# Kernel tuning notes

Measured on AMD Instinct MI355X. Metric: run time of the kernel, lower is better.

Reference implementation:

```python
import jax, jax.numpy as jnp
import numpy as np

N, E, NNZ, CIN, COUT = 100000, 25000, 1600000, 256, 256


def setup_inputs() -> dict:
    key = jax.random.key(0)
    k_x, k_v, k_e, k_w = jax.random.split(key, 4)
    X = jax.random.normal(k_x, (N, CIN), dtype=jnp.float32)
    v_idx = jax.random.randint(k_v, (NNZ,), 0, N)      # vertex of each incidence pair
    e_idx = jax.random.randint(k_e, (NNZ,), 0, E)      # hyperedge of each incidence pair
    # kaiming_normal_ on theta.weight: std = sqrt(2 / fan_in)
    W = jax.random.normal(k_w, (CIN, COUT), dtype=jnp.float32) * np.sqrt(2.0 / CIN)
    b = jnp.zeros((COUT,), dtype=jnp.float32)
    return {"X": X, "W": W, "b": b, "v_idx": v_idx, "e_idx": e_idx}


def reference(X, W, b, v_idx, e_idx):
    # theta: linear projection
    Xp = X @ W + b  # [N, COUT]

    # degrees (edge weights = 1)
    ones = jnp.ones((NNZ,), dtype=Xp.dtype)
    dv = jax.ops.segment_sum(ones, v_idx, num_segments=N)  # vertex degree
    de = jax.ops.segment_sum(ones, e_idx, num_segments=E)  # hyperedge degree
    dv_isqrt = jnp.where(dv > 0, jax.lax.rsqrt(jnp.maximum(dv, 1.0)), 0.0)
    de_inv = jnp.where(de > 0, 1.0 / jnp.maximum(de, 1.0), 0.0)

    # smoothing_with_HGNN: D_v^{-1/2} H D_e^{-1} H^T D_v^{-1/2} Xp
    Xs = Xp * dv_isqrt[:, None]                                            # [N, C]
    Ye = jax.ops.segment_sum(Xs[v_idx], e_idx, num_segments=E) * de_inv[:, None]  # [E, C]
    Zv = jax.ops.segment_sum(Ye[e_idx], v_idx, num_segments=N) * dv_isqrt[:, None]  # [N, C]

    # not is_last: ReLU; bn is None (use_bn=False); dropout identity at eval
    return jax.nn.relu(Zv)
```

## Files before the change

kernel.cpp:

```cpp
#include <hip/hip_runtime.h>
#include <hip/hip_bf16.h>

#define NV 100000
#define NE 25000
#define NNZ_ 1600000
#define CH 256
#define TS 4096
#define NB_T 391
#define EBINS 196
#define VBINS 196
#define HTOT (196*NB_T)
#define SEGCAP 9216
#define LDSK 264

typedef unsigned int u32;
typedef unsigned short u16;
typedef __attribute__((ext_vector_type(8))) short bf16x8;
typedef __attribute__((ext_vector_type(4))) float f32x4;

__device__ __forceinline__ float bf2f(u16 u){ return __uint_as_float(((u32)u)<<16); }
__device__ __forceinline__ u16 f2bf(float f){ __hip_bfloat16 h = __float2bfloat16(f); return *reinterpret_cast<u16*>(&h); }
__device__ __forceinline__ void acc4(float4& a, ushort4 u){
  a.x += bf2f(u.x); a.y += bf2f(u.y); a.z += bf2f(u.z); a.w += bf2f(u.w);
}

__global__ __launch_bounds__(256) void k_hist(const int* __restrict__ v_idx, const int* __restrict__ e_idx,
                       int* __restrict__ histE, int* __restrict__ histV){
  __shared__ int hE[EBINS], hV[VBINS];
  for (int i=threadIdx.x;i<EBINS;i+=256) hE[i]=0;
  for (int i=threadIdx.x;i<VBINS;i+=256) hV[i]=0;
  __syncthreads();
  int i0 = blockIdx.x*TS;
  int n = min(TS, NNZ_-i0);
  for (int k=threadIdx.x;k<n;k+=256){
    int e = e_idx[i0+k], v = v_idx[i0+k];
    atomicAdd(&hE[e>>7],1);
    atomicAdd(&hV[v>>9],1);
  }
  __syncthreads();
  for (int i=threadIdx.x;i<EBINS;i+=256) histE[i*NB_T+blockIdx.x]=hE[i];
  for (int i=threadIdx.x;i<VBINS;i+=256) histV[i*NB_T+blockIdx.x]=hV[i];
}

__global__ void k_scanA(const int* cnt, int n, int* off, int* bsum){
  __shared__ int buf[1024];
  int i = blockIdx.x*1024 + threadIdx.x;
  int x = (i<n) ? cnt[i] : 0;
  buf[threadIdx.x] = x;
  __syncthreads();
  #pragma unroll
  for (int d=1; d<1024; d<<=1){
    int t = (threadIdx.x>=d) ? buf[threadIdx.x-d] : 0;
    __syncthreads();
    buf[threadIdx.x] += t;
    __syncthreads();
  }
  if (i<n) off[i] = buf[threadIdx.x] - x;
  if (threadIdx.x==1023) bsum[blockIdx.x] = buf[1023];
}

__global__ void k_scanB(int* bsum, int nb){
  __shared__ int buf[128];
  int x = (threadIdx.x<nb) ? bsum[threadIdx.x] : 0;
  buf[threadIdx.x] = x;
  __syncthreads();
  #pragma unroll
  for (int d=1; d<128; d<<=1){
    int t = (threadIdx.x>=d) ? buf[threadIdx.x-d] : 0;
    __syncthreads();
    buf[threadIdx.x] += t;
    __syncthreads();
  }
  if (threadIdx.x<nb) bsum[threadIdx.x] = buf[threadIdx.x] - x;
}

__global__ void k_scanC2(int* off, const int* __restrict__ bsum, int n){
  int i = blockIdx.x*blockDim.x + threadIdx.x;
  if (i<n) off[i] += bsum[i>>10];
}

__global__ __launch_bounds__(256) void k_scat(const int* __restrict__ v_idx, const int* __restrict__ e_idx,
                       const int* __restrict__ baseE, const int* __restrict__ baseV,
                       u32* __restrict__ tmpE, u32* __restrict__ tmpV){
  __shared__ int bE[EBINS], bV[VBINS], cE[EBINS], cV[VBINS];
  for (int i=threadIdx.x;i<EBINS;i+=256){ bE[i]=baseE[i*NB_T+blockIdx.x]; cE[i]=0; }
  for (int i=threadIdx.x;i<VBINS;i+=256){ bV[i]=baseV[i*NB_T+blockIdx.x]; cV[i]=0; }
  __syncthreads();
  int i0 = blockIdx.x*TS;
  int n = min(TS, NNZ_-i0);
  for (int k=threadIdx.x;k<n;k+=256){
    int e = e_idx[i0+k], v = v_idx[i0+k];
    int be = e>>7, bv = v>>9;
    int r  = atomicAdd(&cE[be],1);
    tmpE[bE[be]+r] = ((u32)e<<17) | (u32)v;
    int r2 = atomicAdd(&cV[bv],1);
    tmpV[bV[bv]+r2] = ((u32)v<<15) | (u32)e;
  }
}

__global__ __launch_bounds__(256) void k_seg2e(const int* __restrict__ baseE, const u32* __restrict__ tmpE,
                        int* __restrict__ e_off, int* __restrict__ e_list){
  int seg = blockIdx.x;
  int s0 = baseE[seg*NB_T];
  int s1 = (seg+1<EBINS) ? baseE[(seg+1)*NB_T] : NNZ_;
  int len = s1 - s0;
  __shared__ u32 buf[SEGCAP];
  __shared__ int cnt[128], st[129];
  for (int i=threadIdx.x;i<128;i+=256) cnt[i]=0;
  __syncthreads();
  bool fit = (len <= SEGCAP);
  if (fit){
    for (int i=threadIdx.x;i<len;i+=256){ u32 p=tmpE[s0+i]; buf[i]=p; atomicAdd(&cnt[(p>>17)&127],1); }
  } else {
    for (int i=threadIdx.x;i<len;i+=256){ u32 p=tmpE[s0+i]; atomicAdd(&cnt[(p>>17)&127],1); }
  }
  __syncthreads();
  if (threadIdx.x==0){ int a=0; for (int i=0;i<128;i++){ st[i]=a; a+=cnt[i]; } st[128]=a; }
  __syncthreads();
  for (int i=threadIdx.x;i<128;i+=256){
    int e = seg*128 + i;
    if (e < NE) e_off[e] = s0 + st[i];
  }
  if (seg==EBINS-1 && threadIdx.x==0) e_off[NE] = NNZ_;
  for (int i=threadIdx.x;i<128;i+=256) cnt[i]=0;
  __syncthreads();
  if (fit){
    for (int i=threadIdx.x;i<len;i+=256){
      u32 p=buf[i]; int lb=(p>>17)&127; int r=atomicAdd(&cnt[lb],1);
      e_list[s0+st[lb]+r] = (int)(p & 0x1FFFFu);
    }
  } else {
    for (int i=threadIdx.x;i<len;i+=256){
      u32 p=tmpE[s0+i]; int lb=(p>>17)&127; int r=atomicAdd(&cnt[lb],1);
      e_list[s0+st[lb]+r] = (int)(p & 0x1FFFFu);
    }
  }
}

__global__ __launch_bounds__(256) void k_seg2v(const int* __restrict__ baseV, const u32* __restrict__ tmpV,
                        int* __restrict__ v_off, u16* __restrict__ v_list){
  int seg = blockIdx.x;
  int s0 = baseV[seg*NB_T];
  int s1 = (seg+1<VBINS) ? baseV[(seg+1)*NB_T] : NNZ_;
  int len = s1 - s0;
  __shared__ u32 buf[SEGCAP];
  __shared__ int cnt[512], st[513];
  for (int i=threadIdx.x;i<512;i+=256) cnt[i]=0;
  __syncthreads();
  bool fit = (len <= SEGCAP);
  if (fit){
    for (int i=threadIdx.x;i<len;i+=256){ u32 p=tmpV[s0+i]; buf[i]=p; atomicAdd(&cnt[(p>>15)&511],1); }
  } else {
    for (int i=threadIdx.x;i<len;i+=256){ u32 p=tmpV[s0+i]; atomicAdd(&cnt[(p>>15)&511],1); }
  }
  __syncthreads();
  if (threadIdx.x==0){ int a=0; for (int i=0;i<512;i++){ st[i]=a; a+=cnt[i]; } st[512]=a; }
  __syncthreads();
  for (int i=threadIdx.x;i<512;i+=256){
    int v = seg*512 + i;
    if (v < NV) v_off[v] = s0 + st[i];
  }
  if (seg==VBINS-1 && threadIdx.x==0) v_off[NV] = NNZ_;
  for (int i=threadIdx.x;i<512;i+=256) cnt[i]=0;
  __syncthreads();
  if (fit){
    for (int i=threadIdx.x;i<len;i+=256){
      u32 p=buf[i]; int lb=(p>>15)&511; int r=atomicAdd(&cnt[lb],1);
      v_list[s0+st[lb]+r] = (u16)(p & 0x7FFFu);
    }
  } else {
    for (int i=threadIdx.x;i<len;i+=256){
      u32 p=tmpV[s0+i]; int lb=(p>>15)&511; int r=atomicAdd(&cnt[lb],1);
      v_list[s0+st[lb]+r] = (u16)(p & 0x7FFFu);
    }
  }
}

__global__ void k_dvis(const int* __restrict__ v_off, float* __restrict__ dv_isqrt){
  int v = blockIdx.x*blockDim.x + threadIdx.x;
  if (v < NV){ int d = v_off[v+1]-v_off[v]; dv_isqrt[v] = d>0 ? rsqrtf((float)d) : 0.f; }
}

__global__ void k_xs(const float4* __restrict__ X4, const float* __restrict__ dv_isqrt,
                     ushort4* __restrict__ Xs4){
  int i = blockIdx.x*blockDim.x + threadIdx.x;
  int v = i >> 6;
  float w = dv_isqrt[v];
  float4 x = X4[i];
  ushort4 o;
  o.x = f2bf(x.x*w); o.y = f2bf(x.y*w); o.z = f2bf(x.z*w); o.w = f2bf(x.w*w);
  Xs4[i] = o;
}

__global__ void k_wh(const float* __restrict__ W, u16* __restrict__ Wh){
  __shared__ float tile[16][17];
  int bx=blockIdx.x, by=blockIdx.y;
  int tx=threadIdx.x, ty=threadIdx.y;
  tile[ty][tx] = W[(by*16+ty)*256 + bx*16+tx];
  __syncthreads();
  Wh[(bx*16+ty)*256 + by*16+tx] = f2bf(tile[tx][ty]);
}

__global__ __launch_bounds__(256) void k_tegemm(const int* __restrict__ e_off,
                     const int* __restrict__ e_list, const ushort4* __restrict__ Xs4,
                     const float* __restrict__ dv_isqrt, const u16* __restrict__ Wh,
                     float* __restrict__ tb, u16* __restrict__ Ue){
  __shared__ u16 lds[16][LDSK];
  int t = threadIdx.x, w = t>>6, lane = t&63;
  int e0 = blockIdx.x*16;

  for (int j=0;j<4;++j){
    int e = e0 + w*4 + j;
    int r = w*4 + j;
    float4 a0=make_float4(0,0,0,0), a1=make_float4(0,0,0,0);
    float ts = 0.f;
    if (e < NE){
      int beg = e_off[e], deg = e_off[e+1]-beg;
      int m = 0;
      for (; m+8 <= deg; m += 8){
        int v0=e_list[beg+m+0], v1=e_list[beg+m+1], v2=e_list[beg+m+2], v3=e_list[beg+m+3];
        int v4=e_list[beg+m+4], v5=e_list[beg+m+5], v6=e_list[beg+m+6], v7=e_list[beg+m+7];
        ushort4 u0=Xs4[(v0<<6)+lane], u1=Xs4[(v1<<6)+lane], u2=Xs4[(v2<<6)+lane], u3=Xs4[(v3<<6)+lane];
        ushort4 u4=Xs4[(v4<<6)+lane], u5=Xs4[(v5<<6)+lane], u6=Xs4[(v6<<6)+lane], u7=Xs4[(v7<<6)+lane];
        acc4(a0,u0); acc4(a1,u1); acc4(a0,u2); acc4(a1,u3);
        acc4(a0,u4); acc4(a1,u5); acc4(a0,u6); acc4(a1,u7);
        ts += dv_isqrt[v0]+dv_isqrt[v1]+dv_isqrt[v2]+dv_isqrt[v3]
            + dv_isqrt[v4]+dv_isqrt[v5]+dv_isqrt[v6]+dv_isqrt[v7];
      }
      for (; m<deg; ++m){
        int v = e_list[beg+m];
        ushort4 u = Xs4[(v<<6)+lane];
        acc4(a0,u);
        ts += dv_isqrt[v];
      }
      float dinv = deg>0 ? 1.f/(float)deg : 0.f;
      a0.x=(a0.x+a1.x)*dinv; a0.y=(a0.y+a1.y)*dinv; a0.z=(a0.z+a1.z)*dinv; a0.w=(a0.w+a1.w)*dinv;
      if (lane==0) tb[e] = ts*dinv;
    }
    ushort4 o;
    o.x=f2bf(a0.x); o.y=f2bf(a0.y); o.z=f2bf(a0.z); o.w=f2bf(a0.w);
    *reinterpret_cast<ushort4*>(&lds[r][lane*4]) = o;
  }
  __syncthreads();

  int rr = lane & 15, kg = lane >> 4;
  f32x4 acc0={0,0,0,0}, acc1={0,0,0,0}, acc2={0,0,0,0}, acc3={0,0,0,0};
  #pragma unroll
  for (int s=0; s<8; ++s){
    bf16x8 a = *reinterpret_cast<bf16x8*>(&lds[rr][s*32 + kg*8]);
    const u16* wb = &Wh[(size_t)((w*4)*16 + rr)*256 + s*32 + kg*8];
    bf16x8 b0 = *reinterpret_cast<const bf16x8*>(wb);
    bf16x8 b1 = *reinterpret_cast<const bf16x8*>(wb + 16*256);
    bf16x8 b2 = *reinterpret_cast<const bf16x8*>(wb + 32*256);
    bf16x8 b3 = *reinterpret_cast<const bf16x8*>(wb + 48*256);
    acc0 = __builtin_amdgcn_mfma_f32_16x16x32_bf16(a, b0, acc0, 0,0,0);
    acc1 = __builtin_amdgcn_mfma_f32_16x16x32_bf16(a, b1, acc1, 0,0,0);
    acc2 = __builtin_amdgcn_mfma_f32_16x16x32_bf16(a, b2, acc2, 0,0,0);
    acc3 = __builtin_amdgcn_mfma_f32_16x16x32_bf16(a, b3, acc3, 0,0,0);
  }
  __syncthreads();
  #pragma unroll
  for (int reg=0; reg<4; ++reg){
    int row = kg*4 + reg;
    lds[row][(w*4+0)*16 + rr] = f2bf(acc0[reg]);
    lds[row][(w*4+1)*16 + rr] = f2bf(acc1[reg]);
    lds[row][(w*4+2)*16 + rr] = f2bf(acc2[reg]);
    lds[row][(w*4+3)*16 + rr] = f2bf(acc3[reg]);
  }
  __syncthreads();
  int orow = t>>4, oseg = t&15;
  int e = e0 + orow;
  if (e < NE){
    uint4 d0 = *reinterpret_cast<uint4*>(&lds[orow][oseg*16]);
    uint4 d1 = *reinterpret_cast<uint4*>(&lds[orow][oseg*16+8]);
    *reinterpret_cast<uint4*>(&Ue[(size_t)e*256 + oseg*16])     = d0;
    *reinterpret_cast<uint4*>(&Ue[(size_t)e*256 + oseg*16 + 8]) = d1;
  }
}

__global__ __launch_bounds__(256) void k_zv(const int* __restrict__ v_off, const u16* __restrict__ v_list,
                    const ushort4* __restrict__ Ue4, const float* __restrict__ tb,
                    const float* __restrict__ dv_isqrt, const float4* __restrict__ b4,
                    float4* __restrict__ out4){
  int v = blockIdx.x*4 + (threadIdx.x>>6);
  if (v >= NV) return;
  int lane = threadIdx.x & 63;
  int base = v_off[v];
  int deg = v_off[v+1] - base;
  float4 a0 = make_float4(0,0,0,0), a1 = make_float4(0,0,0,0);
  float sb0 = 0.f, sb1 = 0.f;
  int m = 0;
  for (; m+8 <= deg; m += 8){
    int e0=v_list[base+m+0], e1=v_list[base+m+1], e2=v_list[base+m+2], e3=v_list[base+m+3];
    int e4=v_list[base+m+4], e5=v_list[base+m+5], e6=v_list[base+m+6], e7=v_list[base+m+7];
    ushort4 u0=Ue4[(e0<<6)+lane], u1=Ue4[(e1<<6)+lane], u2=Ue4[(e2<<6)+lane], u3=Ue4[(e3<<6)+lane];
    ushort4 u4=Ue4[(e4<<6)+lane], u5=Ue4[(e5<<6)+lane], u6=Ue4[(e6<<6)+lane], u7=Ue4[(e7<<6)+lane];
    acc4(a0,u0); acc4(a1,u1); acc4(a0,u2); acc4(a1,u3);
    acc4(a0,u4); acc4(a1,u5); acc4(a0,u6); acc4(a1,u7);
    sb0 += tb[e0]+tb[e2]+tb[e4]+tb[e6];
    sb1 += tb[e1]+tb[e3]+tb[e5]+tb[e7];
  }
  for (; m<deg; ++m){
    int e = v_list[base+m];
    ushort4 u = Ue4[(e<<6)+lane];
    acc4(a0,u);
    sb0 += tb[e];
  }
  float4 acc;
  acc.x=a0.x+a1.x; acc.y=a0.y+a1.y; acc.z=a0.z+a1.z; acc.w=a0.w+a1.w;
  float w = dv_isqrt[v];
  float sw = (sb0+sb1)*w;
  float4 bb = b4[lane];
  float4 o;
  o.x = fmaxf(0.f, fmaf(sw, bb.x, acc.x*w));
  o.y = fmaxf(0.f, fmaf(sw, bb.y, acc.y*w));
  o.z = fmaxf(0.f, fmaf(sw, bb.z, acc.z*w));
  o.w = fmaxf(0.f, fmaf(sw, bb.w, acc.w*w));
  out4[(v<<6)+lane] = o;
}

extern "C" void kernel_launch(void* const* d_in, const int* in_sizes, int n_in,
                              void* d_out, int out_size, void* d_ws, size_t ws_size,
                              hipStream_t stream) {
  const float* X = (const float*)d_in[0];
  const float* W = (const float*)d_in[1];
  const float* b = (const float*)d_in[2];
  const int* v_idx = (const int*)d_in[3];
  const int* e_idx = (const int*)d_in[4];
  float* out = (float*)d_out;

  char* p = (char*)d_ws;
  auto alloc = [&](size_t bytes)->void*{
    void* r = (void*)p; p += (bytes + 255) & ~(size_t)255; return r;
  };
  int* histE      = (int*)alloc((size_t)HTOT*4);
  int* histV      = (int*)alloc((size_t)HTOT*4);
  int* bsumE      = (int*)alloc(128*4);
  int* bsumV      = (int*)alloc(128*4);
  int* e_off      = (int*)alloc((size_t)(NE+1)*4);
  int* v_off      = (int*)alloc((size_t)(NV+1)*4);
  float* dv_isqrt = (float*)alloc((size_t)NV*4);
  float* tb       = (float*)alloc((size_t)NE*4);
  u32* tmpE       = (u32*)alloc((size_t)NNZ_*4);
  u32* tmpV       = (u32*)alloc((size_t)NNZ_*4);
  int* e_list     = (int*)alloc((size_t)NNZ_*4);
  u16* v_list     = (u16*)alloc((size_t)NNZ_*2);
  u16* Wh         = (u16*)alloc((size_t)CH*CH*2);
  u16* Ue         = (u16*)tmpE;
  u16* Xs         = (u16*)d_out;

  const int nbS = (HTOT+1023)/1024;

  k_hist<<<NB_T,256,0,stream>>>(v_idx,e_idx,histE,histV);
  k_scanA<<<nbS,1024,0,stream>>>(histE,HTOT,histE,bsumE);
  k_scanA<<<nbS,1024,0,stream>>>(histV,HTOT,histV,bsumV);
  k_scanB<<<1,128,0,stream>>>(bsumE,nbS);
  k_scanB<<<1,128,0,stream>>>(bsumV,nbS);
  k_scanC2<<<(HTOT+255)/256,256,0,stream>>>(histE,bsumE,HTOT);
  k_scanC2<<<(HTOT+255)/256,256,0,stream>>>(histV,bsumV,HTOT);
  k_scat<<<NB_T,256,0,stream>>>(v_idx,e_idx,histE,histV,tmpE,tmpV);
  k_seg2e<<<EBINS,256,0,stream>>>(histE,tmpE,e_off,e_list);
  k_seg2v<<<VBINS,256,0,stream>>>(histV,tmpV,v_off,v_list);

  k_dvis<<<(NV+255)/256,256,0,stream>>>(v_off, dv_isqrt);
  k_xs<<<(NV*64)/256,256,0,stream>>>((const float4*)X, dv_isqrt, (ushort4*)Xs);
  k_wh<<<dim3(16,16),dim3(16,16),0,stream>>>(W, Wh);
  k_tegemm<<<(NE+15)/16,256,0,stream>>>(e_off,e_list,(const ushort4*)Xs,dv_isqrt,Wh,tb,Ue);
  k_zv<<<(NV+3)/4,256,0,stream>>>(v_off,v_list,(const ushort4*)Ue,tb,dv_isqrt,(const float4*)b,(float4*)out);
}
```

Before: 369.7 us.

## Merge paired scan/sort/prep launches, add nontemporal hints, two vertices per wave

Merges the separate E/V scan, segment-sort, degree and weight-convert kernels into combined launches, which cuts the launch count and the idle gaps between small kernels. It adds nontemporal loads and stores for streaming index, X and output traffic. The final gather kernel now has each wave process two vertices at once, so more independent loads are in flight. The cost is higher register pressure in the gather kernel and load imbalance when the two vertices have different degrees.

```diff
diff --git a/kernel.cpp b/kernel.cpp
--- a/kernel.cpp
+++ b/kernel.cpp
@@ -33,7 +33,8 @@
   int i0 = blockIdx.x*TS;
   int n = min(TS, NNZ_-i0);
   for (int k=threadIdx.x;k<n;k+=256){
-    int e = e_idx[i0+k], v = v_idx[i0+k];
+    int e = __builtin_nontemporal_load(&e_idx[i0+k]);
+    int v = __builtin_nontemporal_load(&v_idx[i0+k]);
     atomicAdd(&hE[e>>7],1);
     atomicAdd(&hV[v>>9],1);
   }
@@ -42,10 +43,16 @@
   for (int i=threadIdx.x;i<VBINS;i+=256) histV[i*NB_T+blockIdx.x]=hV[i];
 }
 
-__global__ void k_scanA(const int* cnt, int n, int* off, int* bsum){
+__global__ void k_scanA2(int* __restrict__ histE, int* __restrict__ histV,
+                         int* __restrict__ bsumE, int* __restrict__ bsumV){
   __shared__ int buf[1024];
-  int i = blockIdx.x*1024 + threadIdx.x;
-  int x = (i<n) ? cnt[i] : 0;
+  int half = gridDim.x >> 1;
+  int sel = blockIdx.x >= half;
+  int blk = sel ? blockIdx.x - half : blockIdx.x;
+  int* data = sel ? histV : histE;
+  int* bsum = sel ? bsumV : bsumE;
+  int i = blk*1024 + threadIdx.x;
+  int x = (i<HTOT) ? data[i] : 0;
   buf[threadIdx.x] = x;
   __syncthreads();
   #pragma unroll
@@ -55,28 +62,35 @@
     buf[threadIdx.x] += t;
     __syncthreads();
   }
-  if (i<n) off[i] = buf[threadIdx.x] - x;
-  if (threadIdx.x==1023) bsum[blockIdx.x] = buf[1023];
-}
-
-__global__ void k_scanB(int* bsum, int nb){
-  __shared__ int buf[128];
-  int x = (threadIdx.x<nb) ? bsum[threadIdx.x] : 0;
-  buf[threadIdx.x] = x;
+  if (i<HTOT) data[i] = buf[threadIdx.x] - x;
+  if (threadIdx.x==1023) bsum[blk] = buf[1023];
+}
+
+__global__ void k_scanB2(int* __restrict__ bsumE, int* __restrict__ bsumV, int nb){
+  __shared__ int bufE[128], bufV[128];
+  int tid = threadIdx.x;
+  int isV = tid >= 128;
+  int* bsum = isV ? bsumV : bsumE;
+  int* buf  = isV ? bufV  : bufE;
+  int t = tid & 127;
+  int x = (t<nb) ? bsum[t] : 0;
+  buf[t] = x;
   __syncthreads();
   #pragma unroll
   for (int d=1; d<128; d<<=1){
-    int t = (threadIdx.x>=d) ? buf[threadIdx.x-d] : 0;
-    __syncthreads();
-    buf[threadIdx.x] += t;
-    __syncthreads();
-  }
-  if (threadIdx.x<nb) bsum[threadIdx.x] = buf[threadIdx.x] - x;
-}
-
-__global__ void k_scanC2(int* off, const int* __restrict__ bsum, int n){
+    int tmp = (t>=d) ? buf[t-d] : 0;
+    __syncthreads();
+    buf[t] += tmp;
+    __syncthreads();
+  }
+  if (t<nb) bsum[t] = buf[t] - x;
+}
+
+__global__ void k_scanC2(int* __restrict__ histE, int* __restrict__ histV,
+                         const int* __restrict__ bsumE, const int* __restrict__ bsumV){
   int i = blockIdx.x*blockDim.x + threadIdx.x;
-  if (i<n) off[i] += bsum[i>>10];
+  if (i < HTOT) histE[i] += bsumE[i>>10];
+  else if (i < 2*HTOT){ int j = i-HTOT; histV[j] += bsumV[j>>10]; }
 }
 
 __global__ __launch_bounds__(256) void k_scat(const int* __restrict__ v_idx, const int* __restrict__ e_idx,
@@ -89,7 +103,8 @@
   int i0 = blockIdx.x*TS;
   int n = min(TS, NNZ_-i0);
   for (int k=threadIdx.x;k<n;k+=256){
-    int e = e_idx[i0+k], v = v_idx[i0+k];
+    int e = __builtin_nontemporal_load(&e_idx[i0+k]);
+    int v = __builtin_nontemporal_load(&v_idx[i0+k]);
     int be = e>>7, bv = v>>9;
     int r  = atomicAdd(&cE[be],1);
     tmpE[bE[be]+r] = ((u32)e<<17) | (u32)v;
@@ -98,107 +113,109 @@
   }
 }
 
-__global__ __launch_bounds__(256) void k_seg2e(const int* __restrict__ baseE, const u32* __restrict__ tmpE,
-                        int* __restrict__ e_off, int* __restrict__ e_list){
-  int seg = blockIdx.x;
-  int s0 = baseE[seg*NB_T];
-  int s1 = (seg+1<EBINS) ? baseE[(seg+1)*NB_T] : NNZ_;
-  int len = s1 - s0;
-  __shared__ u32 buf[SEGCAP];
-  __shared__ int cnt[128], st[129];
-  for (int i=threadIdx.x;i<128;i+=256) cnt[i]=0;
-  __syncthreads();
-  bool fit = (len <= SEGCAP);
-  if (fit){
-    for (int i=threadIdx.x;i<len;i+=256){ u32 p=tmpE[s0+i]; buf[i]=p; atomicAdd(&cnt[(p>>17)&127],1); }
-  } else {
-    for (int i=threadIdx.x;i<len;i+=256){ u32 p=tmpE[s0+i]; atomicAdd(&cnt[(p>>17)&127],1); }
-  }
-  __syncthreads();
-  if (threadIdx.x==0){ int a=0; for (int i=0;i<128;i++){ st[i]=a; a+=cnt[i]; } st[128]=a; }
-  __syncthreads();
-  for (int i=threadIdx.x;i<128;i+=256){
-    int e = seg*128 + i;
-    if (e < NE) e_off[e] = s0 + st[i];
-  }
-  if (seg==EBINS-1 && threadIdx.x==0) e_off[NE] = NNZ_;
-  for (int i=threadIdx.x;i<128;i+=256) cnt[i]=0;
-  __syncthreads();
-  if (fit){
-    for (int i=threadIdx.x;i<len;i+=256){
-      u32 p=buf[i]; int lb=(p>>17)&127; int r=atomicAdd(&cnt[lb],1);
-      e_list[s0+st[lb]+r] = (int)(p & 0x1FFFFu);
-    }
-  } else {
-    for (int i=threadIdx.x;i<len;i+=256){
-      u32 p=tmpE[s0+i]; int lb=(p>>17)&127; int r=atomicAdd(&cnt[lb],1);
-      e_list[s0+st[lb]+r] = (int)(p & 0x1FFFFu);
-    }
-  }
-}
-
-__global__ __launch_bounds__(256) void k_seg2v(const int* __restrict__ baseV, const u32* __restrict__ tmpV,
+__global__ __launch_bounds__(256) void k_seg2(const int* __restrict__ baseE, const u32* __restrict__ tmpE,
+                        int* __restrict__ e_off, int* __restrict__ e_list,
+                        const int* __restrict__ baseV, const u32* __restrict__ tmpV,
                         int* __restrict__ v_off, u16* __restrict__ v_list){
-  int seg = blockIdx.x;
-  int s0 = baseV[seg*NB_T];
-  int s1 = (seg+1<VBINS) ? baseV[(seg+1)*NB_T] : NNZ_;
-  int len = s1 - s0;
   __shared__ u32 buf[SEGCAP];
   __shared__ int cnt[512], st[513];
-  for (int i=threadIdx.x;i<512;i+=256) cnt[i]=0;
-  __syncthreads();
-  bool fit = (len <= SEGCAP);
-  if (fit){
-    for (int i=threadIdx.x;i<len;i+=256){ u32 p=tmpV[s0+i]; buf[i]=p; atomicAdd(&cnt[(p>>15)&511],1); }
+  if (blockIdx.x < EBINS){
+    int seg = blockIdx.x;
+    int s0 = baseE[seg*NB_T];
+    int s1 = (seg+1<EBINS) ? baseE[(seg+1)*NB_T] : NNZ_;
+    int len = s1 - s0;
+    for (int i=threadIdx.x;i<128;i+=256) cnt[i]=0;
+    __syncthreads();
+    bool fit = (len <= SEGCAP);
+    if (fit){
+      for (int i=threadIdx.x;i<len;i+=256){ u32 p=tmpE[s0+i]; buf[i]=p; atomicAdd(&cnt[(p>>17)&127],1); }
+    } else {
+      for (int i=threadIdx.x;i<len;i+=256){ u32 p=tmpE[s0+i]; atomicAdd(&cnt[(p>>17)&127],1); }
+    }
+    __syncthreads();
+    if (threadIdx.x==0){ int a=0; for (int i=0;i<128;i++){ st[i]=a; a+=cnt[i]; } st[128]=a; }
+    __syncthreads();
+    for (int i=threadIdx.x;i<128;i+=256){
+      int e = seg*128 + i;
+      if (e < NE) e_off[e] = s0 + st[i];
+    }
+    if (seg==EBINS-1 && threadIdx.x==0) e_off[NE] = NNZ_;
+    for (int i=threadIdx.x;i<128;i+=256) cnt[i]=0;
+    __syncthreads();
+    if (fit){
+      for (int i=threadIdx.x;i<len;i+=256){
+        u32 p=buf[i]; int lb=(p>>17)&127; int r=atomicAdd(&cnt[lb],1);
+        e_list[s0+st[lb]+r] = (int)(p & 0x1FFFFu);
+      }
+    } else {
+      for (int i=threadIdx.x;i<len;i+=256){
+        u32 p=tmpE[s0+i]; int lb=(p>>17)&127; int r=atomicAdd(&cnt[lb],1);
+        e_list[s0+st[lb]+r] = (int)(p & 0x1FFFFu);
+      }
+    }
   } else {
-    for (int i=threadIdx.x;i<len;i+=256){ u32 p=tmpV[s0+i]; atomicAdd(&cnt[(p>>15)&511],1); }
-  }
-  __syncthreads();
-  if (threadIdx.x==0){ int a=0; for (int i=0;i<512;i++){ st[i]=a; a+=cnt[i]; } st[512]=a; }
-  __syncthreads();
-  for (int i=threadIdx.x;i<512;i+=256){
-    int v = seg*512 + i;
-    if (v < NV) v_off[v] = s0 + st[i];
-  }
-  if (seg==VBINS-1 && threadIdx.x==0) v_off[NV] = NNZ_;
-  for (int i=threadIdx.x;i<512;i+=256) cnt[i]=0;
-  __syncthreads();
-  if (fit){
-    for (int i=threadIdx.x;i<len;i+=256){
-      u32 p=buf[i]; int lb=(p>>15)&511; int r=atomicAdd(&cnt[lb],1);
-      v_list[s0+st[lb]+r] = (u16)(p & 0x7FFFu);
-    }
+    int seg = blockIdx.x - EBINS;
+    int s0 = baseV[seg*NB_T];
+    int s1 = (seg+1<VBINS) ? baseV[(seg+1)*NB_T] : NNZ_;
+    int len = s1 - s0;
+    for (int i=threadIdx.x;i<512;i+=256) cnt[i]=0;
+    __syncthreads();
+    bool fit = (len <= SEGCAP);
+    if (fit){
+      for (int i=threadIdx.x;i<len;i+=256){ u32 p=tmpV[s0+i]; buf[i]=p; atomicAdd(&cnt[(p>>15)&511],1); }
+    } else {
+      for (int i=threadIdx.x;i<len;i+=256){ u32 p=tmpV[s0+i]; atomicAdd(&cnt[(p>>15)&511],1); }
+    }
+    __syncthreads();
+    if (threadIdx.x==0){ int a=0; for (int i=0;i<512;i++){ st[i]=a; a+=cnt[i]; } st[512]=a; }
+    __syncthreads();
+    for (int i=threadIdx.x;i<512;i+=256){
+      int v = seg*512 + i;
+      if (v < NV) v_off[v] = s0 + st[i];
+    }
+    if (seg==VBINS-1 && threadIdx.x==0) v_off[NV] = NNZ_;
+    for (int i=threadIdx.x;i<512;i+=256) cnt[i]=0;
+    __syncthreads();
+    if (fit){
+      for (int i=threadIdx.x;i<len;i+=256){
+        u32 p=buf[i]; int lb=(p>>15)&511; int r=atomicAdd(&cnt[lb],1);
+        v_list[s0+st[lb]+r] = (u16)(p & 0x7FFFu);
+      }
+    } else {
+      for (int i=threadIdx.x;i<len;i+=256){
+        u32 p=tmpV[s0+i]; int lb=(p>>15)&511; int r=atomicAdd(&cnt[lb],1);
+        v_list[s0+st[lb]+r] = (u16)(p & 0x7FFFu);
+      }
+    }
+  }
+}
+
+__global__ void k_prep(const int* __restrict__ v_off, float* __restrict__ dv_isqrt,
+                       const float* __restrict__ W, u16* __restrict__ Wh){
+  const int nb_dv = (NV+255)/256;
+  if ((int)blockIdx.x < nb_dv){
+    int v = blockIdx.x*256 + threadIdx.x;
+    if (v < NV){ int d = v_off[v+1]-v_off[v]; dv_isqrt[v] = d>0 ? rsqrtf((float)d) : 0.f; }
   } else {
-    for (int i=threadIdx.x;i<len;i+=256){
-      u32 p=tmpV[s0+i]; int lb=(p>>15)&511; int r=atomicAdd(&cnt[lb],1);
-      v_list[s0+st[lb]+r] = (u16)(p & 0x7FFFu);
-    }
-  }
-}
-
-__global__ void k_dvis(const int* __restrict__ v_off, float* __restrict__ dv_isqrt){
-  int v = blockIdx.x*blockDim.x + threadIdx.x;
-  if (v < NV){ int d = v_off[v+1]-v_off[v]; dv_isqrt[v] = d>0 ? rsqrtf((float)d) : 0.f; }
-}
-
-__global__ void k_xs(const float4* __restrict__ X4, const float* __restrict__ dv_isqrt,
+    __shared__ float tile[16][17];
+    int idx = blockIdx.x - nb_dv;
+    int bx = idx & 15, by = idx >> 4;
+    int tx = threadIdx.x & 15, ty = threadIdx.x >> 4;
+    tile[ty][tx] = W[(by*16+ty)*256 + bx*16+tx];
+    __syncthreads();
+    Wh[(bx*16+ty)*256 + by*16+tx] = f2bf(tile[tx][ty]);
+  }
+}
+
+__global__ void k_xs(const f32x4* __restrict__ X4, const float* __restrict__ dv_isqrt,
                      ushort4* __restrict__ Xs4){
   int i = blockIdx.x*blockDim.x + threadIdx.x;
   int v = i >> 6;
   float w = dv_isqrt[v];
-  float4 x = X4[i];
+  f32x4 x = __builtin_nontemporal_load(&X4[i]);
   ushort4 o;
-  o.x = f2bf(x.x*w); o.y = f2bf(x.y*w); o.z = f2bf(x.z*w); o.w = f2bf(x.w*w);
+  o.x = f2bf(x[0]*w); o.y = f2bf(x[1]*w); o.z = f2bf(x[2]*w); o.w = f2bf(x[3]*w);
   Xs4[i] = o;
-}
-
-__global__ void k_wh(const float* __restrict__ W, u16* __restrict__ Wh){
-  __shared__ float tile[16][17];
-  int bx=blockIdx.x, by=blockIdx.y;
-  int tx=threadIdx.x, ty=threadIdx.y;
-  tile[ty][tx] = W[(by*16+ty)*256 + bx*16+tx];
-  __syncthreads();
-  Wh[(bx*16+ty)*256 + by*16+tx] = f2bf(tile[tx][ty]);
 }
 
 __global__ __launch_bounds__(256) void k_tegemm(const int* __restrict__ e_off,
@@ -282,41 +299,76 @@
                     const ushort4* __restrict__ Ue4, const float* __restrict__ tb,
                     const float* __restrict__ dv_isqrt, const float4* __restrict__ b4,
                     float4* __restrict__ out4){
-  int v = blockIdx.x*4 + (threadIdx.x>>6);
-  if (v >= NV) return;
-  int lane = threadIdx.x & 63;
-  int base = v_off[v];
-  int deg = v_off[v+1] - base;
-  float4 a0 = make_float4(0,0,0,0), a1 = make_float4(0,0,0,0);
-  float sb0 = 0.f, sb1 = 0.f;
+  int w = threadIdx.x>>6, lane = threadIdx.x&63;
+  int vA = blockIdx.x*8 + w*2;
+  int vB = vA + 1;
+  int baseA = v_off[vA], degA = v_off[vA+1]-baseA;
+  int baseB = v_off[vB], degB = v_off[vB+1]-baseB;
+  const float4 z = make_float4(0,0,0,0);
+  float4 a0=z, a1=z, c0=z, c1=z;
+  float sbA=0.f, sbB=0.f;
+  int mc = min(degA, degB);
   int m = 0;
-  for (; m+8 <= deg; m += 8){
-    int e0=v_list[base+m+0], e1=v_list[base+m+1], e2=v_list[base+m+2], e3=v_list[base+m+3];
-    int e4=v_list[base+m+4], e5=v_list[base+m+5], e6=v_list[base+m+6], e7=v_list[base+m+7];
+  for (; m+8 <= mc; m += 8){
+    int eA0=v_list[baseA+m+0], eA1=v_list[baseA+m+1], eA2=v_list[baseA+m+2], eA3=v_list[baseA+m+3];
+    int eA4=v_list[baseA+m+4], eA5=v_list[baseA+m+5], eA6=v_list[baseA+m+6], eA7=v_list[baseA+m+7];
+    int eB0=v_list[baseB+m+0], eB1=v_list[baseB+m+1], eB2=v_list[baseB+m+2], eB3=v_list[baseB+m+3];
+    int eB4=v_list[baseB+m+4], eB5=v_list[baseB+m+5], eB6=v_list[baseB+m+6], eB7=v_list[baseB+m+7];
+    ushort4 uA0=Ue4[(eA0<<6)+lane], uA1=Ue4[(eA1<<6)+lane], uA2=Ue4[(eA2<<6)+lane], uA3=Ue4[(eA3<<6)+lane];
+    ushort4 uA4=Ue4[(eA4<<6)+lane], uA5=Ue4[(eA5<<6)+lane], uA6=Ue4[(eA6<<6)+lane], uA7=Ue4[(eA7<<6)+lane];
+    ushort4 uB0=Ue4[(eB0<<6)+lane], uB1=Ue4[(eB1<<6)+lane], uB2=Ue4[(eB2<<6)+lane], uB3=Ue4[(eB3<<6)+lane];
+    ushort4 uB4=Ue4[(eB4<<6)+lane], uB5=Ue4[(eB5<<6)+lane], uB6=Ue4[(eB6<<6)+lane], uB7=Ue4[(eB7<<6)+lane];
+    acc4(a0,uA0); acc4(a1,uA1); acc4(a0,uA2); acc4(a1,uA3);
+    acc4(a0,uA4); acc4(a1,uA5); acc4(a0,uA6); acc4(a1,uA7);
+    acc4(c0,uB0); acc4(c1,uB1); acc4(c0,uB2); acc4(c1,uB3);
+    acc4(c0,uB4); acc4(c1,uB5); acc4(c0,uB6); acc4(c1,uB7);
+    sbA += tb[eA0]+tb[eA1]+tb[eA2]+tb[eA3]+tb[eA4]+tb[eA5]+tb[eA6]+tb[eA7];
+    sbB += tb[eB0]+tb[eB1]+tb[eB2]+tb[eB3]+tb[eB4]+tb[eB5]+tb[eB6]+tb[eB7];
+  }
+  int mA = m;
+  for (; mA+8 <= degA; mA += 8){
+    int e0=v_list[baseA+mA+0], e1=v_list[baseA+mA+1], e2=v_list[baseA+mA+2], e3=v_list[baseA+mA+3];
+    int e4=v_list[baseA+mA+4], e5=v_list[baseA+mA+5], e6=v_list[baseA+mA+6], e7=v_list[baseA+mA+7];
     ushort4 u0=Ue4[(e0<<6)+lane], u1=Ue4[(e1<<6)+lane], u2=Ue4[(e2<<6)+lane], u3=Ue4[(e3<<6)+lane];
     ushort4 u4=Ue4[(e4<<6)+lane], u5=Ue4[(e5<<6)+lane], u6=Ue4[(e6<<6)+lane], u7=Ue4[(e7<<6)+lane];
     acc4(a0,u0); acc4(a1,u1); acc4(a0,u2); acc4(a1,u3);
     acc4(a0,u4); acc4(a1,u5); acc4(a0,u6); acc4(a1,u7);
-    sb0 += tb[e0]+tb[e2]+tb[e4]+tb[e6];
-    sb1 += tb[e1]+tb[e3]+tb[e5]+tb[e7];
-  }
-  for (; m<deg; ++m){
-    int e = v_list[base+m];
-    ushort4 u = Ue4[(e<<6)+lane];
-    acc4(a0,u);
-    sb0 += tb[e];
-  }
-  float4 acc;
-  acc.x=a0.x+a1.x; acc.y=a0.y+a1.y; acc.z=a0.z+a1.z; acc.w=a0.w+a1.w;
-  float w = dv_isqrt[v];
-  float sw = (sb0+sb1)*w;
+    sbA += tb[e0]+tb[e1]+tb[e2]+tb[e3]+tb[e4]+tb[e5]+tb[e6]+tb[e7];
+  }
+  for (; mA<degA; ++mA){
+    int e = v_list[baseA+mA];
+    acc4(a0, Ue4[(e<<6)+lane]);
+    sbA += tb[e];
+  }
+  int mB = m;
+  for (; mB+8 <= degB; mB += 8){
+    int e0=v_list[baseB+mB+0], e1=v_list[baseB+mB+1], e2=v_list[baseB+mB+2], e3=v_list[baseB+mB+3];
+    int e4=v_list[baseB+mB+4], e5=v_list[baseB+mB+5], e6=v_list[baseB+mB+6], e7=v_list[baseB+mB+7];
+    ushort4 u0=Ue4[(e0<<6)+lane], u1=Ue4[(e1<<6)+lane], u2=Ue4[(e2<<6)+lane], u3=Ue4[(e3<<6)+lane];
+    ushort4 u4=Ue4[(e4<<6)+lane], u5=Ue4[(e5<<6)+lane], u6=Ue4[(e6<<6)+lane], u7=Ue4[(e7<<6)+lane];
+    acc4(c0,u0); acc4(c1,u1); acc4(c0,u2); acc4(c1,u3);
+    acc4(c0,u4); acc4(c1,u5); acc4(c0,u6); acc4(c1,u7);
+    sbB += tb[e0]+tb[e1]+tb[e2]+tb[e3]+tb[e4]+tb[e5]+tb[e6]+tb[e7];
+  }
+  for (; mB<degB; ++mB){
+    int e = v_list[baseB+mB];
+    acc4(c0, Ue4[(e<<6)+lane]);
+    sbB += tb[e];
+  }
   float4 bb = b4[lane];
-  float4 o;
-  o.x = fmaxf(0.f, fmaf(sw, bb.x, acc.x*w));
-  o.y = fmaxf(0.f, fmaf(sw, bb.y, acc.y*w));
-  o.z = fmaxf(0.f, fmaf(sw, bb.z, acc.z*w));
-  o.w = fmaxf(0.f, fmaf(sw, bb.w, acc.w*w));
-  out4[(v<<6)+lane] = o;
+  float wA = dv_isqrt[vA], wB = dv_isqrt[vB];
+  float swA = sbA*wA, swB = sbB*wB;
+  f32x4 oA, oB;
+  oA[0] = fmaxf(0.f, fmaf(swA, bb.x, (a0.x+a1.x)*wA));
+  oA[1] = fmaxf(0.f, fmaf(swA, bb.y, (a0.y+a1.y)*wA));
+  oA[2] = fmaxf(0.f, fmaf(swA, bb.z, (a0.z+a1.z)*wA));
+  oA[3] = fmaxf(0.f, fmaf(swA, bb.w, (a0.w+a1.w)*wA));
+  oB[0] = fmaxf(0.f, fmaf(swB, bb.x, (c0.x+c1.x)*wB));
+  oB[1] = fmaxf(0.f, fmaf(swB, bb.y, (c0.y+c1.y)*wB));
+  oB[2] = fmaxf(0.f, fmaf(swB, bb.z, (c0.z+c1.z)*wB));
+  oB[3] = fmaxf(0.f, fmaf(swB, bb.w, (c0.w+c1.w)*wB));
+  __builtin_nontemporal_store(oA, (f32x4*)&out4[(vA<<6)+lane]);
+  __builtin_nontemporal_store(oB, (f32x4*)&out4[(vB<<6)+lane]);
 }
 
 extern "C" void kernel_launch(void* const* d_in, const int* in_sizes, int n_in,
@@ -352,19 +404,13 @@
   const int nbS = (HTOT+1023)/1024;
 
   k_hist<<<NB_T,256,0,stream>>>(v_idx,e_idx,histE,histV);
-  k_scanA<<<nbS,1024,0,stream>>>(histE,HTOT,histE,bsumE);
-  k_scanA<<<nbS,1024,0,stream>>>(histV,HTOT,histV,bsumV);
-  k_scanB<<<1,128,0,stream>>>(bsumE,nbS);
-  k_scanB<<<1,128,0,stream>>>(bsumV,nbS);
-  k_scanC2<<<(HTOT+255)/256,256,0,stream>>>(histE,bsumE,HTOT);
-  k_scanC2<<<(HTOT+255)/256,256,0,stream>>>(histV,bsumV,HTOT);
+  k_scanA2<<<2*nbS,1024,0,stream>>>(histE,histV,bsumE,bsumV);
+  k_scanB2<<<1,256,0,stream>>>(bsumE,bsumV,nbS);
+  k_scanC2<<<(2*HTOT+255)/256,256,0,stream>>>(histE,histV,bsumE,bsumV);
   k_scat<<<NB_T,256,0,stream>>>(v_idx,e_idx,histE,histV,tmpE,tmpV);
-  k_seg2e<<<EBINS,256,0,stream>>>(histE,tmpE,e_off,e_list);
-  k_seg2v<<<VBINS,256,0,stream>>>(histV,tmpV,v_off,v_list);
-
-  k_dvis<<<(NV+255)/256,256,0,stream>>>(v_off, dv_isqrt);
-  k_xs<<<(NV*64)/256,256,0,stream>>>((const float4*)X, dv_isqrt, (ushort4*)Xs);
-  k_wh<<<dim3(16,16),dim3(16,16),0,stream>>>(W, Wh);
+  k_seg2<<<EBINS+VBINS,256,0,stream>>>(histE,tmpE,e_off,e_list,histV,tmpV,v_off,v_list);
+  k_prep<<<(NV+255)/256 + 256,256,0,stream>>>(v_off,dv_isqrt,W,Wh);
+  k_xs<<<(NV*64)/256,256,0,stream>>>((const f32x4*)X, dv_isqrt, (ushort4*)Xs);
   k_tegemm<<<(NE+15)/16,256,0,stream>>>(e_off,e_list,(const ushort4*)Xs,dv_isqrt,Wh,tb,Ue);
-  k_zv<<<(NV+3)/4,256,0,stream>>>(v_off,v_list,(const ushort4*)Ue,tb,dv_isqrt,(const float4*)b,(float4*)out);
-}
+  k_zv<<<NV/8,256,0,stream>>>(v_off,v_list,(const ushort4*)Ue,tb,dv_isqrt,(const float4*)b,(float4*)out);
+}
```

Result: slower. 401.1 us (+8.5%).
